# Kernel tuning notes

Hardware: AMD Instinct MI355X
Metric: run time of the kernel (lower is better)

## Reference

```python
import jax, jax.numpy as jnp
import numpy as np

B, D, H, K = 4096, 768, 16384, 32


def setup_inputs() -> dict:
    key = jax.random.key(0)
    k1, k2, k3 = jax.random.split(key, 3)
    return {
        "x": jax.random.normal(k1, (B, D), dtype=jnp.float32),
        "W_enc": jax.random.normal(k2, (H, D), dtype=jnp.float32) * 0.02,
        "b_enc": jnp.zeros((H,), dtype=jnp.float32),
        "W_dec": jax.random.normal(k3, (D, H), dtype=jnp.float32) * 0.02,
        "b_dec": jnp.zeros((D,), dtype=jnp.float32),
        "k": K,
    }


def reference(x, W_enc, b_enc, W_dec, b_dec, k):
    # Encode: z = ReLU(x W_enc^T + b_enc)   -> [B, H]
    z = jax.nn.relu(jnp.einsum("bd,hd->bh", x, W_enc) + b_enc)
    # Top-k mask along hidden dim (k < H)
    _, topk_idx = jax.lax.top_k(z, k)                      # [B, k]
    rows = jnp.arange(z.shape[0])[:, None]                 # [B, 1]
    mask = jnp.zeros_like(z).at[rows, topk_idx].set(1.0)   # scatter ones
    z = z * mask
    # Decode: x_hat = z W_dec^T + b_dec     -> [B, D]
    x_hat = jnp.einsum("bh,dh->bd", z, W_dec) + b_dec
    return (x_hat, z)
```

## Files before the change

### kernel.cpp

```cpp
#include <hip/hip_runtime.h>

constexpr int NB = 4096;
constexpr int ND = 768;
constexpr int NH = 16384;
constexpr int NK = 32;
constexpr int CAND_MAX = 512;
#define DELTA 0.04f

typedef __bf16 bf16x8 __attribute__((ext_vector_type(8)));
typedef float  f32x4  __attribute__((ext_vector_type(4)));

constexpr size_t OFF_XBF   = 0;
constexpr size_t OFF_WENCB = OFF_XBF   + (size_t)NB * ND * 2;
constexpr size_t OFF_WDECT = OFF_WENCB + (size_t)NH * ND * 2;
constexpr size_t OFF_CIDX  = OFF_WDECT + (size_t)NH * ND * 4;
constexpr size_t OFF_CCNT  = OFF_CIDX  + (size_t)NB * CAND_MAX * 4;
constexpr size_t OFF_ZA    = OFF_CCNT  + (size_t)NB * 4;
constexpr size_t ZA_BYTES  = (size_t)NB * NH * 2;

__device__ inline unsigned short f2bf(float f) {
  unsigned u = __float_as_uint(f);
  unsigned r = u + 0x7fffu + ((u >> 16) & 1u);
  return (unsigned short)(r >> 16);
}

__device__ __forceinline__ void gld_lds16(const unsigned short* g, unsigned short* s) {
  __builtin_amdgcn_global_load_lds((const __attribute__((address_space(1))) void*)g,
                                   (__attribute__((address_space(3))) void*)s, 16, 0, 0);
}

__global__ __launch_bounds__(256) void cast_bf16_kernel(const float* __restrict__ in,
                                                        unsigned short* __restrict__ out,
                                                        int n4) {
  int stride = gridDim.x * 256;
  for (int i = blockIdx.x * 256 + threadIdx.x; i < n4; i += stride) {
    float4 v = ((const float4*)in)[i];
    unsigned long long p = (unsigned long long)f2bf(v.x)
                         | ((unsigned long long)f2bf(v.y) << 16)
                         | ((unsigned long long)f2bf(v.z) << 32)
                         | ((unsigned long long)f2bf(v.w) << 48);
    ((unsigned long long*)out)[i] = p;
  }
}

__global__ __launch_bounds__(256) void transpose_kernel(const float* __restrict__ in,
                                                        float* __restrict__ out) {
  __shared__ float tile[32][33];
  int hb = blockIdx.x * 32, db = blockIdx.y * 32;
  int tx = threadIdx.x, ty = threadIdx.y;
#pragma unroll
  for (int i = 0; i < 4; ++i)
    tile[ty + i * 8][tx] = in[(size_t)(db + ty + i * 8) * NH + hb + tx];
  __syncthreads();
#pragma unroll
  for (int i = 0; i < 4; ++i)
    out[(size_t)(hb + ty + i * 8) * ND + db + tx] = tile[tx][ty + i * 8];
}

__global__ __launch_bounds__(256) void encode_gemm_kernel(
    const unsigned short* __restrict__ Abf,
    const unsigned short* __restrict__ Bbf,
    const float* __restrict__ b_enc,
    unsigned short* __restrict__ za) {
  __shared__ __align__(16) unsigned short As[128 * 64];
  __shared__ __align__(16) unsigned short Bs[128 * 64];

  int bid = blockIdx.x;
  int x  = bid & 7;
  int j  = bid >> 3;
  int st = j >> 6;
  int w  = j & 63;
  int g  = st * 8 + x;
  int bm = (g & 3) * 8 + (w & 7);
  int bn = (g >> 2) * 8 + (w >> 3);
  int m0 = bm * 128, n0 = bn * 128;

  int tid = threadIdx.x, wid = tid >> 6, l = tid & 63;
  int wr = wid >> 1, wc = wid & 1;
  int lr = l & 15, lk = l >> 4;

  int srow = l >> 3;
  int scol = (l & 7) ^ srow;

  f32x4 acc[4][4] = {};

  for (int kt = 0; kt < 12; ++kt) {
    __syncthreads();
#pragma unroll
    for (int t = 0; t < 4; ++t) {
      int c = wid * 4 + t;
      gld_lds16(Abf + ((size_t)(m0 + c * 8 + srow) * ND + kt * 64 + scol * 8), &As[c * 512]);
      gld_lds16(Bbf + ((size_t)(n0 + c * 8 + srow) * ND + kt * 64 + scol * 8), &Bs[c * 512]);
    }
    asm volatile("s_waitcnt vmcnt(0)" ::: "memory");
    __syncthreads();
#pragma unroll
    for (int kk = 0; kk < 2; ++kk) {
      bf16x8 af[4], bq[4];
      int u = (kk * 4 + lk) ^ (lr & 7);
#pragma unroll
      for (int i = 0; i < 4; ++i)
        af[i] = *(const bf16x8*)&As[(wr * 64 + i * 16 + lr) * 64 + u * 8];
#pragma unroll
      for (int j2 = 0; j2 < 4; ++j2)
        bq[j2] = *(const bf16x8*)&Bs[(wc * 64 + j2 * 16 + lr) * 64 + u * 8];
#pragma unroll
      for (int i = 0; i < 4; ++i)
#pragma unroll
        for (int j2 = 0; j2 < 4; ++j2)
          acc[i][j2] = __builtin_amdgcn_mfma_f32_16x16x32_bf16(af[i], bq[j2], acc[i][j2], 0, 0, 0);
    }
  }

  __syncthreads();
  unsigned short* ep = (wid < 2) ? &As[wid * 4096] : &Bs[(wid - 2) * 4096];
#pragma unroll
  for (int j2 = 0; j2 < 4; ++j2) {
    float bias = b_enc[n0 + wc * 64 + j2 * 16 + lr];
#pragma unroll
    for (int i = 0; i < 4; ++i) {
#pragma unroll
      for (int q = 0; q < 4; ++q) {
        int row = i * 16 + lk * 4 + q;
        int col = j2 * 16 + lr;
        float v = fmaxf(acc[i][j2][q] + bias, 0.0f);
        ep[row * 64 + (((col >> 3) ^ (row & 7)) * 8) + (col & 7)] = f2bf(v);
      }
    }
  }
  __syncthreads();
#pragma unroll
  for (int t = 0; t < 8; ++t) {
    int row = t * 8 + (l >> 3);
    int u = (l & 7) ^ (row & 7);
    int4 d = *(const int4*)&ep[row * 64 + u * 8];
    *(int4*)(za + (size_t)(m0 + wr * 64 + row) * NH + n0 + wc * 64 + (l & 7) * 8) = d;
  }
}


__device__ __forceinline__ float bisect_thr(const uint4* v, int* wcnt, int tid) {
  unsigned lo = 0u, hi = 0x7F80u;
  for (int it = 0; it < 15; ++it) {
    unsigned mid = (lo + hi) >> 1;
    int c = 0;
#pragma unroll
    for (int i = 0; i < 8; ++i) {
      const unsigned* p = (const unsigned*)&v[i];
#pragma unroll
      for (int e = 0; e < 4; ++e) {
        unsigned u = p[e];
        c += ((u & 0xFFFFu) >= mid) ? 1 : 0;
        c += ((u >> 16) >= mid) ? 1 : 0;
      }
    }
#pragma unroll
    for (int off = 32; off; off >>= 1) c += __shfl_xor(c, off, 64);
    if ((tid & 63) == 0) wcnt[tid >> 6] = c;
    __syncthreads();
    int tot = wcnt[0] + wcnt[1] + wcnt[2] + wcnt[3];
    __syncthreads();
    if (tot >= NK) {
      lo = mid;
      if (tot <= 48) break;
    } else {
      hi = mid;
    }
  }
  float thr = __uint_as_float(lo << 16) - DELTA;
  return (thr < 1e-12f) ? 1e-12f : thr;
}

__device__ __forceinline__ void topk_wave0(const float* cv, const int* ci, int cnt,
                                           float* sv, int* si, int l) {
  float lv[8]; int lh[8];
#pragma unroll
  for (int ii = 0; ii < 8; ++ii) {
    int c = l + 64 * ii;
    if (c < cnt) { lv[ii] = cv[c]; lh[ii] = ci[c]; }
    else         { lv[ii] = -1.f;  lh[ii] = 0x7fffffff; }
  }
  for (int r = 0; r < NK; ++r) {
    float bv = -1.f; int bh = 0x7fffffff; int bl = l; int bii = 0;
#pragma unroll
    for (int ii = 0; ii < 8; ++ii)
      if (lv[ii] > bv || (lv[ii] == bv && lh[ii] < bh)) { bv = lv[ii]; bh = lh[ii]; bii = ii; }
#pragma unroll
    for (int off = 32; off; off >>= 1) {
      float ov = __shfl_xor(bv, off, 64);
      int   oh = __shfl_xor(bh, off, 64);
      int   ol = __shfl_xor(bl, off, 64);
      int   oi = __shfl_xor(bii, off, 64);
      if (ov > bv || (ov == bv && oh < bh)) { bv = ov; bh = oh; bl = ol; bii = oi; }
    }
    if (l == 0) {
      if (bv > -0.5f) { sv[r] = bv; si[r] = bh; }
      else            { sv[r] = 0.f; si[r] = -1; }
    }
#pragma unroll
    for (int ii = 0; ii < 8; ++ii)
      if (ii == bii && l == bl && bv > -0.5f) lv[ii] = -1.f;
  }
}

__global__ __launch_bounds__(256) void select_kernel(const unsigned short* __restrict__ za,
                                                     int* __restrict__ cand_idx,
                                                     int* __restrict__ cand_cnt) {
  int b = blockIdx.x, tid = threadIdx.x;
  const uint4* zrow = (const uint4*)(za + (size_t)b * NH);
  uint4 v[8];
#pragma unroll
  for (int i = 0; i < 8; ++i) v[i] = zrow[tid + 256 * i];

  __shared__ int wcnt[4];
  __shared__ int lcnt;
  float thr = bisect_thr(v, wcnt, tid);
  if (tid == 0) lcnt = 0;
  __syncthreads();
#pragma unroll
  for (int i = 0; i < 8; ++i) {
    const unsigned* p = (const unsigned*)&v[i];
#pragma unroll
    for (int e = 0; e < 4; ++e) {
      unsigned u = p[e];
      int hbase = (tid + 256 * i) * 8 + e * 2;
      float f0 = __uint_as_float((u & 0xFFFFu) << 16);
      float f1 = __uint_as_float(u & 0xFFFF0000u);
      if (f0 >= thr) { int s = atomicAdd(&lcnt, 1); if (s < CAND_MAX) cand_idx[(size_t)b * CAND_MAX + s] = hbase; }
      if (f1 >= thr) { int s = atomicAdd(&lcnt, 1); if (s < CAND_MAX) cand_idx[(size_t)b * CAND_MAX + s] = hbase + 1; }
    }
  }
  __syncthreads();
  if (tid == 0) cand_cnt[b] = (lcnt < CAND_MAX) ? lcnt : CAND_MAX;
}

__device__ __forceinline__ void finalize_core(
    int b, int tid, int wid, int l, int cnt,
    const float* __restrict__ W_enc, const float* __restrict__ b_enc,
    const float* __restrict__ WdecT, const float* __restrict__ b_dec,
    const float* xr, float* cv, const int* ci, float* sv, int* si,
    float* __restrict__ zout, float* __restrict__ xhat) {
  const float4* xr4 = (const float4*)xr;
  for (int c = wid; c < cnt; c += 4) {
    int h = ci[c];
    const float4* wrow4 = (const float4*)(W_enc + (size_t)h * ND);
    float4 s4 = make_float4(0.f, 0.f, 0.f, 0.f);
#pragma unroll
    for (int i = 0; i < 3; ++i) {
      float4 wv = wrow4[l + 64 * i];
      float4 xv = xr4[l + 64 * i];
      s4.x = fmaf(wv.x, xv.x, s4.x);
      s4.y = fmaf(wv.y, xv.y, s4.y);
      s4.z = fmaf(wv.z, xv.z, s4.z);
      s4.w = fmaf(wv.w, xv.w, s4.w);
    }
    float s = (s4.x + s4.y) + (s4.z + s4.w);
#pragma unroll
    for (int off = 32; off; off >>= 1) s += __shfl_xor(s, off, 64);
    if (l == 0) cv[c] = fmaxf(s + b_enc[h], 0.f);
  }
  __syncthreads();

  if (wid == 0) {
    topk_wave0(cv, ci, cnt, sv, si, l);
  } else {
    float4 z4 = make_float4(0.f, 0.f, 0.f, 0.f);
    float4* zr = (float4*)(zout + (size_t)b * NH);
    for (int i = tid - 64; i < NH / 4; i += 192) zr[i] = z4;
  }
  __syncthreads();

  if (tid < NK) {
    int s = si[tid];
    if (s >= 0) zout[(size_t)b * NH + s] = sv[tid];
  }

  if (tid < ND / 4) {
    float4 a = ((const float4*)b_dec)[tid];
#pragma unroll 8
    for (int j = 0; j < NK; ++j) {
      int hj = si[j]; hj = (hj < 0) ? 0 : hj;
      float vj = sv[j];
      float4 wv = ((const float4*)(WdecT + (size_t)hj * ND))[tid];
      a.x = fmaf(vj, wv.x, a.x);
      a.y = fmaf(vj, wv.y, a.y);
      a.z = fmaf(vj, wv.z, a.z);
      a.w = fmaf(vj, wv.w, a.w);
    }
    ((float4*)(xhat + (size_t)b * ND))[tid] = a;
  }
}

__global__ __launch_bounds__(256) void finalize_kernel(
    const float* __restrict__ x, const float* __restrict__ W_enc,
    const float* __restrict__ b_enc,
    const int* __restrict__ cand_idx, const int* __restrict__ cand_cnt,
    const float* __restrict__ WdecT, const float* __restrict__ b_dec,
    float* __restrict__ zout, float* __restrict__ xhat) {
  int b = blockIdx.x, tid = threadIdx.x;
  int wid = tid >> 6, l = tid & 63;
  __shared__ __align__(16) float xr[ND];
  __shared__ float cv[CAND_MAX];
  __shared__ int   ci[CAND_MAX];
  __shared__ float sv[NK];
  __shared__ int   si[NK];

  int cnt = cand_cnt[b];
  const float4* xrow = (const float4*)(x + (size_t)b * ND);
  for (int i = tid; i < ND / 4; i += 256) ((float4*)xr)[i] = xrow[i];
  for (int c = tid; c < cnt; c += 256) ci[c] = cand_idx[(size_t)b * CAND_MAX + c];
  __syncthreads();
  finalize_core(b, tid, wid, l, cnt, W_enc, b_enc, WdecT, b_dec,
                xr, cv, ci, sv, si, zout, xhat);
}

__global__ __launch_bounds__(256) void fused_finalize_kernel(
    const unsigned short* __restrict__ za,
    const float* __restrict__ x, const float* __restrict__ W_enc,
    const float* __restrict__ b_enc,
    const float* __restrict__ WdecT, const float* __restrict__ b_dec,
    float* __restrict__ zout, float* __restrict__ xhat) {
  int b = blockIdx.x, tid = threadIdx.x;
  int wid = tid >> 6, l = tid & 63;
  __shared__ __align__(16) float xr[ND];
  __shared__ float cv[CAND_MAX];
  __shared__ int   ci[CAND_MAX];
  __shared__ float sv[NK];
  __shared__ int   si[NK];
  __shared__ int   wcnt[4];
  __shared__ int   lcnt;

  const uint4* zrow = (const uint4*)(za + (size_t)b * NH);
  uint4 v[8];
#pragma unroll
  for (int i = 0; i < 8; ++i) v[i] = zrow[tid + 256 * i];
  const float4* xrow = (const float4*)(x + (size_t)b * ND);
  for (int i = tid; i < ND / 4; i += 256) ((float4*)xr)[i] = xrow[i];

  float thr = bisect_thr(v, wcnt, tid);
  if (tid == 0) lcnt = 0;
  __syncthreads();
#pragma unroll
  for (int i = 0; i < 8; ++i) {
    const unsigned* p = (const unsigned*)&v[i];
#pragma unroll
    for (int e = 0; e < 4; ++e) {
      unsigned u = p[e];
      int hbase = (tid + 256 * i) * 8 + e * 2;
      float f0 = __uint_as_float((u & 0xFFFFu) << 16);
      float f1 = __uint_as_float(u & 0xFFFF0000u);
      if (f0 >= thr) { int s = atomicAdd(&lcnt, 1); if (s < CAND_MAX) ci[s] = hbase; }
      if (f1 >= thr) { int s = atomicAdd(&lcnt, 1); if (s < CAND_MAX) ci[s] = hbase + 1; }
    }
  }
  __syncthreads();
  int cnt = (lcnt < CAND_MAX) ? lcnt : CAND_MAX;

  finalize_core(b, tid, wid, l, cnt, W_enc, b_enc, WdecT, b_dec,
                xr, cv, ci, sv, si, zout, xhat);
}

extern "C" void kernel_launch(void* const* d_in, const int* in_sizes, int n_in,
                              void* d_out, int out_size, void* d_ws, size_t ws_size,
                              hipStream_t stream) {
  const float* x     = (const float*)d_in[0];
  const float* W_enc = (const float*)d_in[1];
  const float* b_enc = (const float*)d_in[2];
  const float* W_dec = (const float*)d_in[3];
  const float* b_dec = (const float*)d_in[4];

  float* xhat = (float*)d_out;
  float* zout = (float*)d_out + (size_t)NB * ND;

  char* ws = (char*)d_ws;
  unsigned short* x_bf    = (unsigned short*)(ws + OFF_XBF);
  unsigned short* wenc_bf = (unsigned short*)(ws + OFF_WENCB);
  float*          wdecT   = (float*)(ws + OFF_WDECT);
  int*            cidx    = (int*)(ws + OFF_CIDX);
  int*            ccnt    = (int*)(ws + OFF_CCNT);

  bool fused = ws_size >= OFF_ZA + ZA_BYTES;
  unsigned short* za = fused ? (unsigned short*)(ws + OFF_ZA)
                             : (unsigned short*)zout;

  cast_bf16_kernel<<<1024, 256, 0, stream>>>(x, x_bf, NB * ND / 4);
  cast_bf16_kernel<<<2048, 256, 0, stream>>>(W_enc, wenc_bf, NH * ND / 4);
  transpose_kernel<<<dim3(NH / 32, ND / 32), dim3(32, 8), 0, stream>>>(W_dec, wdecT);
  encode_gemm_kernel<<<(NB / 128) * (NH / 128), 256, 0, stream>>>(x_bf, wenc_bf, b_enc, za);
  if (fused) {
    fused_finalize_kernel<<<NB, 256, 0, stream>>>(za, x, W_enc, b_enc, wdecT, b_dec, zout, xhat);
  } else {
    select_kernel<<<NB, 256, 0, stream>>>(za, cidx, ccnt);
    finalize_kernel<<<NB, 256, 0, stream>>>(x, W_enc, b_enc, cidx, ccnt, wdecT, b_dec, zout, xhat);
  }
}
```

Measured before the change: 401.1 us.

## Restructure encode GEMM into 256x256 tiles with triple-buffered LDS pipeline

The encode GEMM moves from 128x128 tiles with 256 threads to 256x256 tiles with 512 threads and a K step of 32. Global-to-LDS loads now go through a three-stage ring buffer, issued in halves between the MFMA groups, with partial vmcnt waits instead of a full drain every iteration. It also raises MFMA priority with s_setprio and writes the epilogue in two halves. The aim is to hide load latency and improve operand reuse, at the cost of 96KB LDS per block, more registers and lower occupancy.

```diff
diff --git a/kernel.cpp b/kernel.cpp
--- a/kernel.cpp
+++ b/kernel.cpp
@@ -57,84 +57,131 @@
     out[(size_t)(hb + ty + i * 8) * ND + db + tx] = tile[tx][ty + i * 8];
 }
 
-__global__ __launch_bounds__(256) void encode_gemm_kernel(
+__global__ __launch_bounds__(512) void encode_gemm_kernel(
     const unsigned short* __restrict__ Abf,
     const unsigned short* __restrict__ Bbf,
     const float* __restrict__ b_enc,
     unsigned short* __restrict__ za) {
-  __shared__ __align__(16) unsigned short As[128 * 64];
-  __shared__ __align__(16) unsigned short Bs[128 * 64];
+  __shared__ __align__(16) unsigned short lds_all[3 * 16384];
 
   int bid = blockIdx.x;
-  int x  = bid & 7;
-  int j  = bid >> 3;
-  int st = j >> 6;
-  int w  = j & 63;
-  int g  = st * 8 + x;
-  int bm = (g & 3) * 8 + (w & 7);
-  int bn = (g >> 2) * 8 + (w >> 3);
-  int m0 = bm * 128, n0 = bn * 128;
-
-  int tid = threadIdx.x, wid = tid >> 6, l = tid & 63;
-  int wr = wid >> 1, wc = wid & 1;
+  int xx = bid & 7;
+  int jj = bid >> 3;
+  int st = jj >> 4;
+  int w  = jj & 15;
+  int g  = st * 8 + xx;
+  int bm = (g & 3) * 4 + (w & 3);
+  int bn = (g >> 2) * 4 + (w >> 2);
+  int m0 = bm * 256, n0 = bn * 256;
+
+  int tid = threadIdx.x;
+  int wid = tid >> 6, l = tid & 63;
+  int wr = wid >> 2, wc = wid & 3;
   int lr = l & 15, lk = l >> 4;
 
-  int srow = l >> 3;
-  int scol = (l & 7) ^ srow;
-
-  f32x4 acc[4][4] = {};
-
-  for (int kt = 0; kt < 12; ++kt) {
+#define STAGE_A(nbuf, ktile, t) do {                                              \
+    int c_ = (t) * 512 + tid; int r_ = c_ >> 2;                                   \
+    int lu_ = (c_ & 3) ^ ((r_ >> 1) & 3);                                         \
+    gld_lds16(Abf + (size_t)(m0 + r_) * ND + (ktile) * 32 + lu_ * 8,              \
+              lds_all + (nbuf) * 16384 + ((t) * 512 + (wid << 6)) * 8);           \
+  } while (0)
+#define STAGE_B(nbuf, ktile, t) do {                                              \
+    int c_ = (t) * 512 + tid; int r_ = c_ >> 2;                                   \
+    int lu_ = (c_ & 3) ^ ((r_ >> 1) & 3);                                         \
+    gld_lds16(Bbf + (size_t)(n0 + r_) * ND + (ktile) * 32 + lu_ * 8,              \
+              lds_all + (nbuf) * 16384 + 8192 + ((t) * 512 + (wid << 6)) * 8);    \
+  } while (0)
+
+  f32x4 acc[8][4] = {};
+
+  STAGE_A(0, 0, 0); STAGE_A(0, 0, 1); STAGE_B(0, 0, 0); STAGE_B(0, 0, 1);
+  STAGE_A(1, 1, 0); STAGE_A(1, 1, 1); STAGE_B(1, 1, 0); STAGE_B(1, 1, 1);
+  asm volatile("s_waitcnt vmcnt(4)" ::: "memory");
+  __builtin_amdgcn_s_barrier();
+  __builtin_amdgcn_sched_barrier(0);
+
+  int cur = 0;
+  for (int kt = 0; kt < 24; ++kt) {
+    int nx = cur + 2; if (nx >= 3) nx -= 3;
+    const unsigned short* Ab = lds_all + cur * 16384;
+    const unsigned short* Bb = Ab + 8192;
+    bf16x8 aF[4], bF[4];
+
+#pragma unroll
+    for (int fj = 0; fj < 4; ++fj) {
+      int row = wc * 64 + fj * 16 + lr;
+      int pu = lk ^ ((row >> 1) & 3);
+      bF[fj] = *(const bf16x8*)(Bb + row * 32 + pu * 8);
+    }
+#pragma unroll
+    for (int fi = 0; fi < 4; ++fi) {
+      int row = wr * 128 + fi * 16 + lr;
+      int pu = lk ^ ((row >> 1) & 3);
+      aF[fi] = *(const bf16x8*)(Ab + row * 32 + pu * 8);
+    }
+    if (kt < 22) { STAGE_A(nx, kt + 2, 0); STAGE_A(nx, kt + 2, 1); }
+    __builtin_amdgcn_s_setprio(1);
+#pragma unroll
+    for (int fi = 0; fi < 4; ++fi)
+#pragma unroll
+      for (int fj = 0; fj < 4; ++fj)
+        acc[fi][fj] = __builtin_amdgcn_mfma_f32_16x16x32_bf16(aF[fi], bF[fj], acc[fi][fj], 0, 0, 0);
+    __builtin_amdgcn_s_setprio(0);
+
+#pragma unroll
+    for (int fi = 0; fi < 4; ++fi) {
+      int row = wr * 128 + (4 + fi) * 16 + lr;
+      int pu = lk ^ ((row >> 1) & 3);
+      aF[fi] = *(const bf16x8*)(Ab + row * 32 + pu * 8);
+    }
+    if (kt < 22) { STAGE_B(nx, kt + 2, 0); STAGE_B(nx, kt + 2, 1); }
+    __builtin_amdgcn_s_setprio(1);
+#pragma unroll
+    for (int fi = 0; fi < 4; ++fi)
+#pragma unroll
+      for (int fj = 0; fj < 4; ++fj)
+        acc[4 + fi][fj] = __builtin_amdgcn_mfma_f32_16x16x32_bf16(aF[fi], bF[fj], acc[4 + fi][fj], 0, 0, 0);
+    __builtin_amdgcn_s_setprio(0);
+
+    if (kt < 23) {
+      if (kt == 22) asm volatile("s_waitcnt vmcnt(0)" ::: "memory");
+      else          asm volatile("s_waitcnt vmcnt(4)" ::: "memory");
+      __builtin_amdgcn_s_barrier();
+      __builtin_amdgcn_sched_barrier(0);
+    }
+    cur = (cur == 2) ? 0 : cur + 1;
+  }
+#undef STAGE_A
+#undef STAGE_B
+
+  __syncthreads();
+  unsigned short* ep = lds_all + wid * 4096;
+#pragma unroll
+  for (int half = 0; half < 2; ++half) {
+#pragma unroll
+    for (int fj = 0; fj < 4; ++fj) {
+      float bias = b_enc[n0 + wc * 64 + fj * 16 + lr];
+#pragma unroll
+      for (int i2 = 0; i2 < 4; ++i2) {
+#pragma unroll
+        for (int q = 0; q < 4; ++q) {
+          int row = i2 * 16 + lk * 4 + q;
+          int col = fj * 16 + lr;
+          float v = fmaxf(acc[half * 4 + i2][fj][q] + bias, 0.0f);
+          ep[row * 64 + (((col >> 3) ^ (row & 7)) * 8) + (col & 7)] = f2bf(v);
+        }
+      }
+    }
     __syncthreads();
 #pragma unroll
-    for (int t = 0; t < 4; ++t) {
-      int c = wid * 4 + t;
-      gld_lds16(Abf + ((size_t)(m0 + c * 8 + srow) * ND + kt * 64 + scol * 8), &As[c * 512]);
-      gld_lds16(Bbf + ((size_t)(n0 + c * 8 + srow) * ND + kt * 64 + scol * 8), &Bs[c * 512]);
-    }
-    asm volatile("s_waitcnt vmcnt(0)" ::: "memory");
+    for (int t = 0; t < 8; ++t) {
+      int row = t * 8 + (l >> 3);
+      int u = (l & 7) ^ (row & 7);
+      int4 d = *(const int4*)&ep[row * 64 + u * 8];
+      *(int4*)(za + (size_t)(m0 + wr * 128 + half * 64 + row) * NH
+                    + n0 + wc * 64 + (l & 7) * 8) = d;
+    }
     __syncthreads();
-#pragma unroll
-    for (int kk = 0; kk < 2; ++kk) {
-      bf16x8 af[4], bq[4];
-      int u = (kk * 4 + lk) ^ (lr & 7);
-#pragma unroll
-      for (int i = 0; i < 4; ++i)
-        af[i] = *(const bf16x8*)&As[(wr * 64 + i * 16 + lr) * 64 + u * 8];
-#pragma unroll
-      for (int j2 = 0; j2 < 4; ++j2)
-        bq[j2] = *(const bf16x8*)&Bs[(wc * 64 + j2 * 16 + lr) * 64 + u * 8];
-#pragma unroll
-      for (int i = 0; i < 4; ++i)
-#pragma unroll
-        for (int j2 = 0; j2 < 4; ++j2)
-          acc[i][j2] = __builtin_amdgcn_mfma_f32_16x16x32_bf16(af[i], bq[j2], acc[i][j2], 0, 0, 0);
-    }
-  }
-
-  __syncthreads();
-  unsigned short* ep = (wid < 2) ? &As[wid * 4096] : &Bs[(wid - 2) * 4096];
-#pragma unroll
-  for (int j2 = 0; j2 < 4; ++j2) {
-    float bias = b_enc[n0 + wc * 64 + j2 * 16 + lr];
-#pragma unroll
-    for (int i = 0; i < 4; ++i) {
-#pragma unroll
-      for (int q = 0; q < 4; ++q) {
-        int row = i * 16 + lk * 4 + q;
-        int col = j2 * 16 + lr;
-        float v = fmaxf(acc[i][j2][q] + bias, 0.0f);
-        ep[row * 64 + (((col >> 3) ^ (row & 7)) * 8) + (col & 7)] = f2bf(v);
-      }
-    }
-  }
-  __syncthreads();
-#pragma unroll
-  for (int t = 0; t < 8; ++t) {
-    int row = t * 8 + (l >> 3);
-    int u = (l & 7) ^ (row & 7);
-    int4 d = *(const int4*)&ep[row * 64 + u * 8];
-    *(int4*)(za + (size_t)(m0 + wr * 64 + row) * NH + n0 + wc * 64 + (l & 7) * 8) = d;
   }
 }
 
@@ -386,7 +433,7 @@
   cast_bf16_kernel<<<1024, 256, 0, stream>>>(x, x_bf, NB * ND / 4);
   cast_bf16_kernel<<<2048, 256, 0, stream>>>(W_enc, wenc_bf, NH * ND / 4);
   transpose_kernel<<<dim3(NH / 32, ND / 32), dim3(32, 8), 0, stream>>>(W_dec, wdecT);
-  encode_gemm_kernel<<<(NB / 128) * (NH / 128), 256, 0, stream>>>(x_bf, wenc_bf, b_enc, za);
+  encode_gemm_kernel<<<(NB / 256) * (NH / 256), 512, 0, stream>>>(x_bf, wenc_bf, b_enc, za);
   if (fused) {
     fused_finalize_kernel<<<NB, 256, 0, stream>>>(za, x, W_enc, b_enc, wdecT, b_dec, zout, xhat);
   } else {
```

Result: faster. 358.3 us (-10.7%).
